# Kernel tuning notes

Hardware: AMD Instinct MI355X
Metric: run time of the kernel (lower is better)

The kernel has to match this reference:

```python
import jax, jax.numpy as jnp
import numpy as np

# Static sizes (RED-GNN on ICEWS14-like graph)
B = 32          # batch (queries)
N = 100000      # active nodes per layer (fixed frontier size)
E = 1000000     # edges per layer
H = 64          # hidden_dim
A = 5           # attn_dim
L = 3           # n_layer
N_REL = 230
N_ENT = 7128
N_TIME = 365


def setup_inputs() -> dict:
    key = jax.random.key(0)
    ks = jax.random.split(key, 16)
    inp = {}
    # edge structure (constant w.r.t. differentiation)
    inp['batch_idx'] = jax.random.randint(ks[0], (E,), 0, B)
    inp['src_idx'] = jax.random.randint(ks[1], (E,), 0, N)
    inp['dst_idx'] = jax.random.randint(ks[2], (E,), 0, N)
    inp['rel_idx'] = jax.random.randint(ks[3], (E,), 0, N_REL + 1)
    # signed relative time in [-(N_TIME-1), N_TIME-1]
    inp['rel_time'] = jax.random.randint(ks[4], (E,), -(N_TIME - 1), N_TIME)
    inp['query_rel'] = jax.random.randint(ks[5], (B,), 0, N_REL + 1)
    # unique (batch, entity) slot per final node
    n = jnp.arange(N)
    inp['out_batch'] = n // N_ENT
    inp['out_ent'] = n % N_ENT
    # learned parameters
    s = 1.0 / np.sqrt(H)
    inp['rela_embed'] = jax.random.normal(ks[6], (L, N_REL + 1, H), jnp.float32) * s
    inp['time_embed'] = jax.random.normal(ks[7], (N_TIME, H), jnp.float32) * s
    inp['Wp'] = jax.random.normal(ks[8], (H, H), jnp.float32) * s
    inp['Wn'] = jax.random.normal(ks[9], (H, H), jnp.float32) * s
    inp['Wf'] = jax.random.normal(ks[10], (H, H), jnp.float32) * s
    inp['W1'] = jax.random.normal(ks[11], (L, A, 3 * H), jnp.float32) * s
    inp['W2'] = jax.random.normal(ks[12], (L, 1, A), jnp.float32) / np.sqrt(A)
    inp['Wc'] = jax.random.normal(ks[13], (1, H), jnp.float32) * s
    inp['bc'] = jnp.zeros((1,), jnp.float32)
    return inp


def reference(rela_embed, time_embed, Wp, Wn, Wf, W1, W2, Wc, bc,
              batch_idx, src_idx, dst_idx, rel_idx, rel_time,
              query_rel, out_batch, out_ent):
    hidden = jnp.zeros((N, H), dtype=rela_embed.dtype)
    q_rel_e = query_rel[batch_idx]                 # [E]
    t_emb = time_embed[jnp.abs(rel_time)]          # [E,H]
    pos = (rel_time > 0)[:, None]
    zer = (rel_time == 0)[:, None]
    for i in range(L):
        rel_e = rela_embed[i][rel_idx]             # [E,H]
        embed = hidden[src_idx] + rel_e + t_emb    # [E,H]
        # branch by sign of relative time: future / now / past linear
        transformed = jnp.where(pos, embed @ Wf.T,
                      jnp.where(zer, embed @ Wn.T, embed @ Wp.T))
        attn_in = jnp.concatenate(
            [hidden[src_idx], rel_e, rela_embed[i][q_rel_e]], axis=1)  # [E,3H]
        score = jax.nn.sigmoid(
            jax.nn.relu(attn_in @ W1[i].T) @ W2[i].T)  # [E,1]
        msg = score * transformed                      # [E,H]
        hidden = jax.nn.relu(
            jax.ops.segment_sum(msg, dst_idx, num_segments=N))
    result = (hidden @ Wc.T + bc).reshape(-1)          # [N]
    score_all = jnp.zeros((B, N_ENT), result.dtype)
    score_all = score_all.at[out_batch, out_ent].set(result)
    return score_all
```

## Files before the change

### kernel.cpp

```cpp
#include <hip/hip_runtime.h>

#define NB   32
#define NN   100000
#define NE   1000000
#define HD   64
#define AD   5
#define NL   3
#define NRL  231
#define NTM  365
#define NOUT 228096
#define NBLK1 391


__device__ __forceinline__ float bflo(unsigned u) { return __uint_as_float(u << 16); }
__device__ __forceinline__ float bfhi(unsigned u) { return __uint_as_float(u & 0xffff0000u); }
__device__ __forceinline__ unsigned packbf2(float x, float y) {
    unsigned ux = __float_as_uint(x), uy = __float_as_uint(y);
    ux = (ux + 0x7fffu + ((ux >> 16) & 1u)) >> 16;
    uy = (uy + 0x7fffu + ((uy >> 16) & 1u)) >> 16;
    return ux | (uy << 16);
}

using vbf8  = __attribute__((ext_vector_type(8))) short;
using f32x4 = __attribute__((ext_vector_type(4))) float;

__global__ __launch_bounds__(256) void prep_wtb_kernel(
    const float* __restrict__ Wp, const float* __restrict__ Wn,
    const float* __restrict__ Wf, ushort* __restrict__ WTB)
{
    int i = blockIdx.x * 256 + threadIdx.x;
    if (i >= 3072) return;
    int lane = i & 63;
    int nt = (i >> 6) & 3;
    int ks = (i >> 8) & 1;
    int hl = (i >> 9) & 1;
    int c  = i >> 10;
    const float* W = (c == 0) ? Wf : (c == 1 ? Wn : Wp);
    int h  = nt * 16 + (lane & 15);
    int k0 = ks * 32 + (lane >> 4) * 8;
    unsigned up[4];
    #pragma unroll
    for (int j = 0; j < 4; ++j) {
        float x = W[h * 64 + k0 + 2 * j];
        float y = W[h * 64 + k0 + 2 * j + 1];
        unsigned pb = packbf2(x, y);
        if (hl) {
            float rx = x - bflo(pb);
            float ry = y - bfhi(pb);
            pb = packbf2(rx, ry);
        }
        up[j] = pb;
    }
    *(uint4*)(WTB + (size_t)i * 8) = make_uint4(up[0], up[1], up[2], up[3]);
}

__global__ __launch_bounds__(256) void prep_tables_kernel(
    const float* __restrict__ rela_embed,
    const float* __restrict__ W1,
    float* __restrict__ Trel,
    float* __restrict__ Tq)
{
    int l = blockIdx.x;
    int r = threadIdx.x;
    if (r >= NRL) return;
    const float4* rrow = (const float4*)(rela_embed + ((size_t)l * NRL + r) * HD);
    const float* W1l = W1 + (size_t)l * AD * 192;
    float tr[AD] = {0,0,0,0,0}, tq[AD] = {0,0,0,0,0};
    #pragma unroll
    for (int k4 = 0; k4 < 16; ++k4) {
        float4 x = rrow[k4];
        #pragma unroll
        for (int a = 0; a < AD; ++a) {
            const float* wr = W1l + a * 192 + 64 + k4 * 4;
            const float* wq = W1l + a * 192 + 128 + k4 * 4;
            tr[a] = fmaf(x.x, wr[0], tr[a]); tr[a] = fmaf(x.y, wr[1], tr[a]);
            tr[a] = fmaf(x.z, wr[2], tr[a]); tr[a] = fmaf(x.w, wr[3], tr[a]);
            tq[a] = fmaf(x.x, wq[0], tq[a]); tq[a] = fmaf(x.y, wq[1], tq[a]);
            tq[a] = fmaf(x.z, wq[2], tq[a]); tq[a] = fmaf(x.w, wq[3], tq[a]);
        }
    }
    float* tro = Trel + ((size_t)l * NRL + r) * 8;
    float* tqo = Tq   + ((size_t)l * NRL + r) * 8;
    #pragma unroll
    for (int a = 0; a < AD; ++a) { tro[a] = tr[a]; tqo[a] = tq[a]; }
    tro[5] = tro[6] = tro[7] = 0.f;
    tqo[5] = tqo[6] = tqo[7] = 0.f;
}

__global__ __launch_bounds__(256) void hist_kernel(
    const int* __restrict__ dst_idx, int* __restrict__ deg,
    ushort* __restrict__ rank)
{
    int e = blockIdx.x * 256 + threadIdx.x;
    if (e < NE) rank[e] = (ushort)atomicAdd(&deg[dst_idx[e]], 1);
}

__global__ __launch_bounds__(256) void scan1_kernel(
    const int* __restrict__ deg, int* __restrict__ tmp, int* __restrict__ bsum)
{
    __shared__ int s[256];
    int tid = threadIdx.x;
    int i = blockIdx.x * 256 + tid;
    int v = (i < NN) ? deg[i] : 0;
    s[tid] = v;
    __syncthreads();
    #pragma unroll
    for (int st = 1; st < 256; st <<= 1) {
        int t = (tid >= st) ? s[tid - st] : 0;
        __syncthreads();
        s[tid] += t;
        __syncthreads();
    }
    if (i < NN) tmp[i] = s[tid];
    if (tid == 255) bsum[blockIdx.x] = s[255];
}

__global__ __launch_bounds__(512) void scan2_kernel(
    const int* __restrict__ bsum, int* __restrict__ bpref)
{
    __shared__ int s[512];
    int tid = threadIdx.x;
    int v = (tid < NBLK1) ? bsum[tid] : 0;
    s[tid] = v;
    __syncthreads();
    #pragma unroll
    for (int st = 1; st < 512; st <<= 1) {
        int t = (tid >= st) ? s[tid - st] : 0;
        __syncthreads();
        s[tid] += t;
        __syncthreads();
    }
    if (tid < NBLK1) bpref[tid] = s[tid] - v;
}

__global__ __launch_bounds__(256) void scan3_kernel(
    const int* __restrict__ deg, const int* __restrict__ tmp,
    const int* __restrict__ bpref, int* __restrict__ off)
{
    int i = blockIdx.x * 256 + threadIdx.x;
    if (i >= NN) return;
    int incl = tmp[i] + bpref[i >> 8];
    off[i + 1] = incl;
    if (i == 0) off[0] = 0;
}

__global__ __launch_bounds__(256) void sort_scatter_kernel(
    const int* __restrict__ dst_idx, const int* __restrict__ src_idx,
    const int* __restrict__ rel_idx, const int* __restrict__ rel_time,
    const int* __restrict__ batch_idx, const int* __restrict__ query_rel,
    const int* __restrict__ off, const ushort* __restrict__ rank,
    const float* __restrict__ Trel0, const float* __restrict__ Tq0,
    const float* __restrict__ W2,
    int2* __restrict__ meta, float* __restrict__ score0)
{
    int e = blockIdx.x * 256 + threadIdx.x;
    if (e >= NE) return;
    int d = dst_idx[e];
    int rt = rel_time[e];
    int cls = (rt > 0) ? 0 : ((rt == 0) ? 1 : 2);
    int ta = (rt < 0) ? -rt : rt;
    int rel = rel_idx[e];
    int q = query_rel[batch_idx[e]];
    int pos = off[d] + (int)rank[e];
    int2 m;
    m.x = src_idx[e] | (rel << 17) | (cls << 25);
    m.y = ta | (q << 9);
    meta[pos] = m;

    float4 t0 = *(const float4*)(Trel0 + rel * 8);
    float  t4 = Trel0[rel * 8 + 4];
    float4 u0 = *(const float4*)(Tq0 + q * 8);
    float  u4 = Tq0[q * 8 + 4];
    float z = 0.f;
    z = fmaf(fmaxf(t0.x + u0.x, 0.f), W2[0], z);
    z = fmaf(fmaxf(t0.y + u0.y, 0.f), W2[1], z);
    z = fmaf(fmaxf(t0.z + u0.z, 0.f), W2[2], z);
    z = fmaf(fmaxf(t0.w + u0.w, 0.f), W2[3], z);
    z = fmaf(fmaxf(t4   + u4,   0.f), W2[4], z);
    score0[pos] = 1.f / (1.f + __expf(-z));
}

__global__ __launch_bounds__(256) void score_kernel(
    const float* __restrict__ proj,
    const float* __restrict__ Trel,
    const float* __restrict__ Tq,
    const float* __restrict__ W2,
    const int2* __restrict__ meta,
    float* __restrict__ score)
{
    int j = blockIdx.x * 256 + threadIdx.x;
    if (j >= NE) return;
    int2 mt = meta[j];
    int rel = (mt.x >> 17) & 0xFF;
    int q   = (mt.y >> 9) & 0xFF;
    int src = mt.x & 0x1FFFF;

    float4 t0 = *(const float4*)(Trel + rel * 8);
    float  t4 = Trel[rel * 8 + 4];
    float4 u0 = *(const float4*)(Tq + q * 8);
    float  u4 = Tq[q * 8 + 4];
    float4 p0 = *(const float4*)(proj + (size_t)src * 8);
    float  p4 = proj[(size_t)src * 8 + 4];
    float z = 0.f;
    z = fmaf(fmaxf(p0.x + t0.x + u0.x, 0.f), W2[0], z);
    z = fmaf(fmaxf(p0.y + t0.y + u0.y, 0.f), W2[1], z);
    z = fmaf(fmaxf(p0.z + t0.z + u0.z, 0.f), W2[2], z);
    z = fmaf(fmaxf(p0.w + t0.w + u0.w, 0.f), W2[3], z);
    z = fmaf(fmaxf(p4   + t4   + u4,   0.f), W2[4], z);
    score[j] = 1.f / (1.f + __expf(-z));
}

template <bool HZ>
__device__ __forceinline__ void edge1(
    int2 m, float sc, int hc8,
    const ushort* __restrict__ hidden_in,
    const float* __restrict__ rela, const float* __restrict__ temb,
    float4* __restrict__ A)
{
    int src = m.x & 0x1FFFF, rel = (m.x >> 17) & 0xFF;
    int cl  = (m.x >> 25) & 3, ta = m.y & 511;
    const float* rp = rela + rel * HD + hc8;
    const float* tp = temb + ta * HD + hc8;
    float4 rv0 = *(const float4*)rp;
    float4 rv1 = *(const float4*)(rp + 4);
    float4 tv0 = *(const float4*)tp;
    float4 tv1 = *(const float4*)(tp + 4);
    float4 v0, v1;
    v0.x = rv0.x + tv0.x; v0.y = rv0.y + tv0.y;
    v0.z = rv0.z + tv0.z; v0.w = rv0.w + tv0.w;
    v1.x = rv1.x + tv1.x; v1.y = rv1.y + tv1.y;
    v1.z = rv1.z + tv1.z; v1.w = rv1.w + tv1.w;
    if (!HZ) {
        uint4 hv = *(const uint4*)(hidden_in + (size_t)src * HD + hc8);
        v0.x += bflo(hv.x); v0.y += bfhi(hv.x);
        v0.z += bflo(hv.y); v0.w += bfhi(hv.y);
        v1.x += bflo(hv.z); v1.y += bfhi(hv.z);
        v1.z += bflo(hv.w); v1.w += bfhi(hv.w);
    }
    float sA = (cl == 0) ? sc : 0.f;
    float sB = (cl == 1) ? sc : 0.f;
    float sC = (cl == 2) ? sc : 0.f;
    A[0].x = fmaf(sA, v0.x, A[0].x); A[0].y = fmaf(sA, v0.y, A[0].y);
    A[0].z = fmaf(sA, v0.z, A[0].z); A[0].w = fmaf(sA, v0.w, A[0].w);
    A[1].x = fmaf(sA, v1.x, A[1].x); A[1].y = fmaf(sA, v1.y, A[1].y);
    A[1].z = fmaf(sA, v1.z, A[1].z); A[1].w = fmaf(sA, v1.w, A[1].w);
    A[2].x = fmaf(sB, v0.x, A[2].x); A[2].y = fmaf(sB, v0.y, A[2].y);
    A[2].z = fmaf(sB, v0.z, A[2].z); A[2].w = fmaf(sB, v0.w, A[2].w);
    A[3].x = fmaf(sB, v1.x, A[3].x); A[3].y = fmaf(sB, v1.y, A[3].y);
    A[3].z = fmaf(sB, v1.z, A[3].z); A[3].w = fmaf(sB, v1.w, A[3].w);
    A[4].x = fmaf(sC, v0.x, A[4].x); A[4].y = fmaf(sC, v0.y, A[4].y);
    A[4].z = fmaf(sC, v0.z, A[4].z); A[4].w = fmaf(sC, v0.w, A[4].w);
    A[5].x = fmaf(sC, v1.x, A[5].x); A[5].y = fmaf(sC, v1.y, A[5].y);
    A[5].z = fmaf(sC, v1.z, A[5].z); A[5].w = fmaf(sC, v1.w, A[5].w);
}

#define SPITCH 68
template <bool HZ, bool PROJ>
__global__ __launch_bounds__(256, 4) void reduce_transform_kernel(
    const ushort* __restrict__ hidden_in,
    const float* __restrict__ rela,
    const float* __restrict__ temb,
    const float* __restrict__ score,
    const int2* __restrict__ meta,
    const int*  __restrict__ off,
    const ushort* __restrict__ WTB,
    const float* __restrict__ W1next,
    ushort* __restrict__ hidden_out,
    float* __restrict__ proj_out)
{
    __shared__ float lds_t[64 * SPITCH];
    int tid  = threadIdx.x;
    int lane = tid & 63;
    int w    = __builtin_amdgcn_readfirstlane(tid >> 6);
    int g    = lane >> 3;
    int hc   = lane & 7;
    int hc8  = hc * 8;
    int node0 = blockIdx.x * 64;
    int h0 = w * 16;

    float4 a[2][6];
    #pragma unroll
    for (int rr = 0; rr < 2; ++rr)
        #pragma unroll
        for (int c = 0; c < 6; ++c)
            a[rr][c] = make_float4(0.f, 0.f, 0.f, 0.f);

    #pragma unroll
    for (int rr = 0; rr < 2; ++rr) {
        int nl = w * 16 + rr * 8 + g;
        int node = node0 + nl;
        if (node >= NN) continue;
        int o0 = off[node];
        int o1 = off[node + 1];
        int j = o0;
        for (; j + 2 <= o1; j += 2) {
            int2 m0 = meta[j], m1 = meta[j + 1];
            float s0 = score[j], s1 = score[j + 1];
            edge1<HZ>(m0, s0, hc8, hidden_in, rela, temb, a[rr]);
            edge1<HZ>(m1, s1, hc8, hidden_in, rela, temb, a[rr]);
        }
        if (j < o1)
            edge1<HZ>(meta[j], score[j], hc8, hidden_in, rela, temb, a[rr]);
    }

    unsigned* lds_u = (unsigned*)lds_t;
    int rl = lane & 15;
    int t  = lane >> 4;
    f32x4 accd[4];
    #pragma unroll
    for (int nt = 0; nt < 4; ++nt)
        accd[nt] = (f32x4){0.f, 0.f, 0.f, 0.f};

    #pragma unroll
    for (int c = 0; c < 3; ++c) {
        __syncthreads();
        #pragma unroll
        for (int rr = 0; rr < 2; ++rr) {
            int nl = w * 16 + rr * 8 + g;
            float4 v0 = a[rr][2 * c];
            float4 v1 = a[rr][2 * c + 1];
            unsigned p0 = packbf2(v0.x, v0.y);
            unsigned p1 = packbf2(v0.z, v0.w);
            unsigned p2 = packbf2(v1.x, v1.y);
            unsigned p3 = packbf2(v1.z, v1.w);
            unsigned q0 = packbf2(v0.x - bflo(p0), v0.y - bfhi(p0));
            unsigned q1 = packbf2(v0.z - bflo(p1), v0.w - bfhi(p1));
            unsigned q2 = packbf2(v1.x - bflo(p2), v1.y - bfhi(p2));
            unsigned q3 = packbf2(v1.z - bflo(p3), v1.w - bfhi(p3));
            *(uint4*)(lds_u + nl * SPITCH + hc * 4)      = make_uint4(p0, p1, p2, p3);
            *(uint4*)(lds_u + nl * SPITCH + 32 + hc * 4) = make_uint4(q0, q1, q2, q3);
        }
        __syncthreads();
        #pragma unroll
        for (int ks = 0; ks < 2; ++ks) {
            const unsigned* rowp = lds_u + (w * 16 + rl) * SPITCH + ks * 16 + t * 4;
            vbf8 ah = *(const vbf8*)rowp;
            vbf8 al = *(const vbf8*)(rowp + 32);
            #pragma unroll
            for (int nt = 0; nt < 4; ++nt) {
                const ushort* bp = WTB +
                    (size_t)((((c * 2) * 2 + ks) * 4 + nt) * 64 + lane) * 8;
                vbf8 bh = *(const vbf8*)bp;
                vbf8 bl = *(const vbf8*)(bp + 4096);
                accd[nt] = __builtin_amdgcn_mfma_f32_16x16x32_bf16(ah, bh, accd[nt], 0, 0, 0);
                accd[nt] = __builtin_amdgcn_mfma_f32_16x16x32_bf16(al, bh, accd[nt], 0, 0, 0);
                accd[nt] = __builtin_amdgcn_mfma_f32_16x16x32_bf16(ah, bl, accd[nt], 0, 0, 0);
            }
        }
    }

    __syncthreads();
    #pragma unroll
    for (int nt = 0; nt < 4; ++nt)
        #pragma unroll
        for (int i = 0; i < 4; ++i)
            lds_t[(w * 16 + t * 4 + i) * SPITCH + nt * 16 + rl] = accd[nt][i];
    __syncthreads();

    float acc[16];
    {
        const float4* rp = (const float4*)(lds_t + lane * SPITCH + h0);
        #pragma unroll
        for (int i4 = 0; i4 < 4; ++i4) {
            float4 v = rp[i4];
            acc[i4 * 4 + 0] = v.x; acc[i4 * 4 + 1] = v.y;
            acc[i4 * 4 + 2] = v.z; acc[i4 * 4 + 3] = v.w;
        }
    }

    int node = node0 + lane;
    if (node < NN) {
        ushort* outp = hidden_out + (size_t)node * 64 + h0;
        unsigned up[8];
        #pragma unroll
        for (int p = 0; p < 8; ++p)
            up[p] = packbf2(fmaxf(acc[2 * p], 0.f), fmaxf(acc[2 * p + 1], 0.f));
        *(uint4*)(outp)     = make_uint4(up[0], up[1], up[2], up[3]);
        *(uint4*)(outp + 8) = make_uint4(up[4], up[5], up[6], up[7]);
    }

    if (PROJ) {
        float pa[AD];
        #pragma unroll
        for (int aa = 0; aa < AD; ++aa) pa[aa] = 0.f;
        #pragma unroll
        for (int i = 0; i < 16; ++i) {
            float hv = fmaxf(acc[i], 0.f);
            #pragma unroll
            for (int aa = 0; aa < AD; ++aa)
                pa[aa] = fmaf(hv, W1next[aa * 192 + h0 + i], pa[aa]);
        }
        __syncthreads();
        float* lds2 = lds_t;
        #pragma unroll
        for (int aa = 0; aa < AD; ++aa)
            lds2[(w * 64 + lane) * AD + aa] = pa[aa];
        __syncthreads();
        for (int idx = tid; idx < 64 * 8; idx += 256) {
            int nd = idx >> 3, aa = idx & 7;
            if (node0 + nd >= NN) break;
            float v = 0.f;
            if (aa < AD) {
                #pragma unroll
                for (int w4 = 0; w4 < 4; ++w4)
                    v += lds2[(w4 * 64 + nd) * AD + aa];
            }
            proj_out[(size_t)(node0 + nd) * 8 + aa] = v;
        }
    }
}

__global__ __launch_bounds__(256) void out_kernel(
    const ushort* __restrict__ hidden,
    const float* __restrict__ Wc,
    const float* __restrict__ bc,
    float* __restrict__ out)
{
    int i = blockIdx.x * 256 + threadIdx.x;
    if (i >= NOUT) return;
    float r = 0.f;
    if (i < NN) {
        const uint4* h4 = (const uint4*)(hidden + (size_t)i * 64);
        float acc = 0.f;
        #pragma unroll
        for (int q = 0; q < 8; ++q) {
            uint4 hv = h4[q];
            const float* wq = Wc + q * 8;
            acc = fmaf(bflo(hv.x), wq[0], acc);
            acc = fmaf(bfhi(hv.x), wq[1], acc);
            acc = fmaf(bflo(hv.y), wq[2], acc);
            acc = fmaf(bfhi(hv.y), wq[3], acc);
            acc = fmaf(bflo(hv.z), wq[4], acc);
            acc = fmaf(bfhi(hv.z), wq[5], acc);
            acc = fmaf(bflo(hv.w), wq[6], acc);
            acc = fmaf(bfhi(hv.w), wq[7], acc);
        }
        r = acc + bc[0];
    }
    out[i] = r;
}

extern "C" void kernel_launch(void* const* d_in, const int* in_sizes, int n_in,
                              void* d_out, int out_size, void* d_ws, size_t ws_size,
                              hipStream_t stream)
{
    const int*   batch_idx  = (const int*)d_in[0];
    const int*   src_idx    = (const int*)d_in[1];
    const int*   dst_idx    = (const int*)d_in[2];
    const int*   rel_idx    = (const int*)d_in[3];
    const int*   rel_time   = (const int*)d_in[4];
    const int*   query_rel  = (const int*)d_in[5];
    const float* rela_embed = (const float*)d_in[8];
    const float* time_embed = (const float*)d_in[9];
    const float* Wp         = (const float*)d_in[10];
    const float* Wn         = (const float*)d_in[11];
    const float* Wf         = (const float*)d_in[12];
    const float* W1         = (const float*)d_in[13];
    const float* W2         = (const float*)d_in[14];
    const float* Wc         = (const float*)d_in[15];
    const float* bc         = (const float*)d_in[16];
    float* out = (float*)d_out;

    char* ws = (char*)d_ws;
    ushort* hid0  = (ushort*)(ws + 0);
    ushort* hid1  = (ushort*)(ws + 12800000);
    float* projA  = (float*)(ws + 25600000);
    float* projB  = (float*)(ws + 28800000);
    float* score  = (float*)(ws + 32000000);
    ushort* WTB   = (ushort*)(ws + 36000000);
    float* Trel   = (float*)(ws + 36100000);
    float* Tq     = (float*)(ws + 36130000);
    int*   off    = (int*)  (ws + 36160000);
    int2*  meta   = (int2*) (ws + 37400000);
    int*   deg    = (int*)  (ws + 45400000);
    int*   tmp    = (int*)  (ws + 46600000);
    ushort* rank  = (ushort*)(ws + 47000000);
    int*   bsum   = (int*)  (ws + 49000000);
    int*   bpref  = (int*)  (ws + 49010000);

    prep_wtb_kernel<<<12, 256, 0, stream>>>(Wp, Wn, Wf, WTB);
    prep_tables_kernel<<<NL, 256, 0, stream>>>(rela_embed, W1, Trel, Tq);

    hipMemsetAsync(deg, 0, NN * sizeof(int), stream);
    hist_kernel<<<(NE + 255) / 256, 256, 0, stream>>>(dst_idx, deg, rank);
    scan1_kernel<<<NBLK1, 256, 0, stream>>>(deg, tmp, bsum);
    scan2_kernel<<<1, 512, 0, stream>>>(bsum, bpref);
    scan3_kernel<<<NBLK1, 256, 0, stream>>>(deg, tmp, bpref, off);
    sort_scatter_kernel<<<(NE + 255) / 256, 256, 0, stream>>>(
        dst_idx, src_idx, rel_idx, rel_time, batch_idx, query_rel,
        off, rank, Trel, Tq, W2, meta, score);

    int grid = (NN + 63) / 64;
    int sgrid = (NE + 255) / 256;
    {
        reduce_transform_kernel<true, true><<<grid, 256, 0, stream>>>(
            hid1, rela_embed, time_embed, score, meta, off,
            WTB, W1 + (size_t)1 * AD * 192, hid0, projA);
    }
    {
        const float* rela = rela_embed + (size_t)1 * NRL * HD;
        score_kernel<<<sgrid, 256, 0, stream>>>(
            projA, Trel + (size_t)1 * NRL * 8, Tq + (size_t)1 * NRL * 8,
            W2 + 1 * AD, meta, score);
        reduce_transform_kernel<false, true><<<grid, 256, 0, stream>>>(
            hid0, rela, time_embed, score, meta, off,
            WTB, W1 + (size_t)2 * AD * 192, hid1, projB);
    }
    {
        const float* rela = rela_embed + (size_t)2 * NRL * HD;
        score_kernel<<<sgrid, 256, 0, stream>>>(
            projB, Trel + (size_t)2 * NRL * 8, Tq + (size_t)2 * NRL * 8,
            W2 + 2 * AD, meta, score);
        reduce_transform_kernel<false, false><<<grid, 256, 0, stream>>>(
            hid1, rela, time_embed, score, meta, off,
            WTB, nullptr, hid0, nullptr);
    }

    out_kernel<<<(NOUT + 255) / 256, 256, 0, stream>>>(hid0, Wc, bc, out);
}
```

Baseline: 397.8 us.

## Shrink reduce-transform blocks to 32 nodes with one node per 8-thread group

Each reduce_transform block now handles 32 nodes instead of 64. Each 8-thread group gathers edges for one node rather than two nodes sequentially. The MFMA transform is split across the four waves as a 2x2 grid of row and column tiles, and the epilogue and projection reduction are remapped to match. The goal is more blocks and more parallelism in the latency-bound edge gather, at the cost of reloading the weight tiles in more blocks and doing fewer MFMAs per wave. It also drops the boundary checks, relying on NN being divisible by 32.

```diff
diff --git a/kernel.cpp b/kernel.cpp
--- a/kernel.cpp
+++ b/kernel.cpp
@@ -10,6 +10,8 @@
 #define NTM  365
 #define NOUT 228096
 #define NBLK1 391
+#define BLKN 32
+#define NBLK2 3125
 
 
 __device__ __forceinline__ float bflo(unsigned u) { return __uint_as_float(u << 16); }
@@ -268,57 +270,50 @@
     ushort* __restrict__ hidden_out,
     float* __restrict__ proj_out)
 {
-    __shared__ float lds_t[64 * SPITCH];
+    __shared__ float lds_t[BLKN * SPITCH];
     int tid  = threadIdx.x;
     int lane = tid & 63;
     int w    = __builtin_amdgcn_readfirstlane(tid >> 6);
-    int g    = lane >> 3;
-    int hc   = lane & 7;
+    int gid  = tid >> 3;
+    int hc   = tid & 7;
     int hc8  = hc * 8;
-    int node0 = blockIdx.x * 64;
-    int h0 = w * 16;
-
-    float4 a[2][6];
-    #pragma unroll
-    for (int rr = 0; rr < 2; ++rr)
-        #pragma unroll
-        for (int c = 0; c < 6; ++c)
-            a[rr][c] = make_float4(0.f, 0.f, 0.f, 0.f);
-
-    #pragma unroll
-    for (int rr = 0; rr < 2; ++rr) {
-        int nl = w * 16 + rr * 8 + g;
-        int node = node0 + nl;
-        if (node >= NN) continue;
+    int node0 = blockIdx.x * BLKN;
+    int node  = node0 + gid;
+
+    float4 a[6];
+    #pragma unroll
+    for (int c = 0; c < 6; ++c)
+        a[c] = make_float4(0.f, 0.f, 0.f, 0.f);
+
+    {
         int o0 = off[node];
         int o1 = off[node + 1];
         int j = o0;
         for (; j + 2 <= o1; j += 2) {
             int2 m0 = meta[j], m1 = meta[j + 1];
             float s0 = score[j], s1 = score[j + 1];
-            edge1<HZ>(m0, s0, hc8, hidden_in, rela, temb, a[rr]);
-            edge1<HZ>(m1, s1, hc8, hidden_in, rela, temb, a[rr]);
+            edge1<HZ>(m0, s0, hc8, hidden_in, rela, temb, a);
+            edge1<HZ>(m1, s1, hc8, hidden_in, rela, temb, a);
         }
         if (j < o1)
-            edge1<HZ>(meta[j], score[j], hc8, hidden_in, rela, temb, a[rr]);
+            edge1<HZ>(meta[j], score[j], hc8, hidden_in, rela, temb, a);
     }
 
     unsigned* lds_u = (unsigned*)lds_t;
     int rl = lane & 15;
     int t  = lane >> 4;
-    f32x4 accd[4];
-    #pragma unroll
-    for (int nt = 0; nt < 4; ++nt)
-        accd[nt] = (f32x4){0.f, 0.f, 0.f, 0.f};
+    int rt = w & 1;
+    int ct = w >> 1;
+    f32x4 accd[2];
+    accd[0] = (f32x4){0.f, 0.f, 0.f, 0.f};
+    accd[1] = (f32x4){0.f, 0.f, 0.f, 0.f};
 
     #pragma unroll
     for (int c = 0; c < 3; ++c) {
         __syncthreads();
-        #pragma unroll
-        for (int rr = 0; rr < 2; ++rr) {
-            int nl = w * 16 + rr * 8 + g;
-            float4 v0 = a[rr][2 * c];
-            float4 v1 = a[rr][2 * c + 1];
+        {
+            float4 v0 = a[2 * c];
+            float4 v1 = a[2 * c + 1];
             unsigned p0 = packbf2(v0.x, v0.y);
             unsigned p1 = packbf2(v0.z, v0.w);
             unsigned p2 = packbf2(v1.x, v1.y);
@@ -327,56 +322,52 @@
             unsigned q1 = packbf2(v0.z - bflo(p1), v0.w - bfhi(p1));
             unsigned q2 = packbf2(v1.x - bflo(p2), v1.y - bfhi(p2));
             unsigned q3 = packbf2(v1.z - bflo(p3), v1.w - bfhi(p3));
-            *(uint4*)(lds_u + nl * SPITCH + hc * 4)      = make_uint4(p0, p1, p2, p3);
-            *(uint4*)(lds_u + nl * SPITCH + 32 + hc * 4) = make_uint4(q0, q1, q2, q3);
+            *(uint4*)(lds_u + gid * SPITCH + hc * 4)      = make_uint4(p0, p1, p2, p3);
+            *(uint4*)(lds_u + gid * SPITCH + 32 + hc * 4) = make_uint4(q0, q1, q2, q3);
         }
         __syncthreads();
         #pragma unroll
         for (int ks = 0; ks < 2; ++ks) {
-            const unsigned* rowp = lds_u + (w * 16 + rl) * SPITCH + ks * 16 + t * 4;
+            const unsigned* rowp = lds_u + (rt * 16 + rl) * SPITCH + ks * 16 + t * 4;
             vbf8 ah = *(const vbf8*)rowp;
             vbf8 al = *(const vbf8*)(rowp + 32);
             #pragma unroll
-            for (int nt = 0; nt < 4; ++nt) {
+            for (int b = 0; b < 2; ++b) {
+                int nt = ct * 2 + b;
                 const ushort* bp = WTB +
                     (size_t)((((c * 2) * 2 + ks) * 4 + nt) * 64 + lane) * 8;
                 vbf8 bh = *(const vbf8*)bp;
                 vbf8 bl = *(const vbf8*)(bp + 4096);
-                accd[nt] = __builtin_amdgcn_mfma_f32_16x16x32_bf16(ah, bh, accd[nt], 0, 0, 0);
-                accd[nt] = __builtin_amdgcn_mfma_f32_16x16x32_bf16(al, bh, accd[nt], 0, 0, 0);
-                accd[nt] = __builtin_amdgcn_mfma_f32_16x16x32_bf16(ah, bl, accd[nt], 0, 0, 0);
+                accd[b] = __builtin_amdgcn_mfma_f32_16x16x32_bf16(ah, bh, accd[b], 0, 0, 0);
+                accd[b] = __builtin_amdgcn_mfma_f32_16x16x32_bf16(al, bh, accd[b], 0, 0, 0);
+                accd[b] = __builtin_amdgcn_mfma_f32_16x16x32_bf16(ah, bl, accd[b], 0, 0, 0);
             }
         }
     }
 
     __syncthreads();
     #pragma unroll
-    for (int nt = 0; nt < 4; ++nt)
+    for (int b = 0; b < 2; ++b)
         #pragma unroll
         for (int i = 0; i < 4; ++i)
-            lds_t[(w * 16 + t * 4 + i) * SPITCH + nt * 16 + rl] = accd[nt][i];
+            lds_t[(rt * 16 + t * 4 + i) * SPITCH + (ct * 2 + b) * 16 + rl] = accd[b][i];
     __syncthreads();
 
-    float acc[16];
+    float acc8[8];
     {
-        const float4* rp = (const float4*)(lds_t + lane * SPITCH + h0);
-        #pragma unroll
-        for (int i4 = 0; i4 < 4; ++i4) {
-            float4 v = rp[i4];
-            acc[i4 * 4 + 0] = v.x; acc[i4 * 4 + 1] = v.y;
-            acc[i4 * 4 + 2] = v.z; acc[i4 * 4 + 3] = v.w;
-        }
-    }
-
-    int node = node0 + lane;
-    if (node < NN) {
-        ushort* outp = hidden_out + (size_t)node * 64 + h0;
-        unsigned up[8];
-        #pragma unroll
-        for (int p = 0; p < 8; ++p)
-            up[p] = packbf2(fmaxf(acc[2 * p], 0.f), fmaxf(acc[2 * p + 1], 0.f));
-        *(uint4*)(outp)     = make_uint4(up[0], up[1], up[2], up[3]);
-        *(uint4*)(outp + 8) = make_uint4(up[4], up[5], up[6], up[7]);
+        const float4* rp = (const float4*)(lds_t + gid * SPITCH + hc8);
+        float4 x = rp[0], y = rp[1];
+        acc8[0] = x.x; acc8[1] = x.y; acc8[2] = x.z; acc8[3] = x.w;
+        acc8[4] = y.x; acc8[5] = y.y; acc8[6] = y.z; acc8[7] = y.w;
+    }
+
+    {
+        ushort* outp = hidden_out + (size_t)node * 64 + hc8;
+        unsigned u0 = packbf2(fmaxf(acc8[0], 0.f), fmaxf(acc8[1], 0.f));
+        unsigned u1 = packbf2(fmaxf(acc8[2], 0.f), fmaxf(acc8[3], 0.f));
+        unsigned u2 = packbf2(fmaxf(acc8[4], 0.f), fmaxf(acc8[5], 0.f));
+        unsigned u3 = packbf2(fmaxf(acc8[6], 0.f), fmaxf(acc8[7], 0.f));
+        *(uint4*)outp = make_uint4(u0, u1, u2, u3);
     }
 
     if (PROJ) {
@@ -384,29 +375,26 @@
         #pragma unroll
         for (int aa = 0; aa < AD; ++aa) pa[aa] = 0.f;
         #pragma unroll
-        for (int i = 0; i < 16; ++i) {
-            float hv = fmaxf(acc[i], 0.f);
+        for (int i = 0; i < 8; ++i) {
+            float hv = fmaxf(acc8[i], 0.f);
             #pragma unroll
             for (int aa = 0; aa < AD; ++aa)
-                pa[aa] = fmaf(hv, W1next[aa * 192 + h0 + i], pa[aa]);
+                pa[aa] = fmaf(hv, W1next[aa * 192 + hc8 + i], pa[aa]);
         }
         __syncthreads();
         float* lds2 = lds_t;
         #pragma unroll
         for (int aa = 0; aa < AD; ++aa)
-            lds2[(w * 64 + lane) * AD + aa] = pa[aa];
-        __syncthreads();
-        for (int idx = tid; idx < 64 * 8; idx += 256) {
-            int nd = idx >> 3, aa = idx & 7;
-            if (node0 + nd >= NN) break;
-            float v = 0.f;
-            if (aa < AD) {
-                #pragma unroll
-                for (int w4 = 0; w4 < 4; ++w4)
-                    v += lds2[(w4 * 64 + nd) * AD + aa];
-            }
-            proj_out[(size_t)(node0 + nd) * 8 + aa] = v;
-        }
+            lds2[tid * AD + aa] = pa[aa];
+        __syncthreads();
+        int nd = tid >> 3, aa = tid & 7;
+        float v = 0.f;
+        if (aa < AD) {
+            #pragma unroll
+            for (int ho = 0; ho < 8; ++ho)
+                v += lds2[(nd * 8 + ho) * AD + aa];
+        }
+        proj_out[(size_t)(node0 + nd) * 8 + aa] = v;
     }
 }
 
@@ -490,7 +478,7 @@
         dst_idx, src_idx, rel_idx, rel_time, batch_idx, query_rel,
         off, rank, Trel, Tq, W2, meta, score);
 
-    int grid = (NN + 63) / 64;
+    int grid = NBLK2;
     int sgrid = (NE + 255) / 256;
     {
         reduce_transform_kernel<true, true><<<grid, 256, 0, stream>>>(
```

Result: no change. 394.6 us (-0.8%).
